# Kernel tuning notes

Hardware: AMD Instinct MI355X
Metric: run time of the kernel (lower is better)

The kernel has to match this reference:

```python
import jax, jax.numpy as jnp
import numpy as np

N_NODES = 50000
N_EDGES = 800000
IN_DIM = 128
OUT_DIM = 128
NEG_SLOPE = 0.01  # F.leaky_relu default


def setup_inputs() -> dict:
    key = jax.random.key(0)
    k_h, k_src, k_dst, k_w, k_as, k_ad = jax.random.split(key, 6)
    h = jax.random.normal(k_h, (N_NODES, IN_DIM), dtype=jnp.float32)
    src = jax.random.randint(k_src, (N_EDGES,), 0, N_NODES, dtype=jnp.int32)
    dst = jax.random.randint(k_dst, (N_EDGES,), 0, N_NODES, dtype=jnp.int32)
    # fc weight: xavier_normal with relu gain; stored as [in, out] for h @ W
    gain = float(np.sqrt(2.0))
    std_w = gain * np.sqrt(2.0 / (IN_DIM + OUT_DIM))
    W = jax.random.normal(k_w, (IN_DIM, OUT_DIM), dtype=jnp.float32) * std_w
    # attn weight [1, 2*out] split into src/dst halves (concat@a == z_s@a_s + z_d@a_d)
    std_a = gain * np.sqrt(2.0 / (2 * OUT_DIM + 1))
    a_src = jax.random.normal(k_as, (OUT_DIM,), dtype=jnp.float32) * std_a
    a_dst = jax.random.normal(k_ad, (OUT_DIM,), dtype=jnp.float32) * std_a
    return {"h": h, "src": src, "dst": dst, "W": W, "a_src": a_src, "a_dst": a_dst}


def reference(h, src, dst, W, a_src, a_dst):
    n = h.shape[0]
    z = h @ W                                   # [N, D]
    # edge attention: leaky_relu(attn(concat[z_src, z_dst]))
    e = z[src] @ a_src + z[dst] @ a_dst         # [E]
    e = jnp.where(e >= 0, e, NEG_SLOPE * e)
    # segment softmax over incoming edges of each dst node
    m = jax.ops.segment_max(e, dst, num_segments=n)    # [N]
    m = jnp.where(jnp.isfinite(m), m, 0.0)             # guard zero-in-degree nodes
    ex = jnp.exp(e - m[dst])                            # [E]
    denom = jax.ops.segment_sum(ex, dst, num_segments=n)
    denom = jnp.where(denom > 0, denom, 1.0)
    alpha = ex / denom[dst]                             # [E]
    # weighted scatter-sum of source features
    out = jax.ops.segment_sum(alpha[:, None] * z[src], dst, num_segments=n)  # [N, D]
    return out
```

## Files before the change

### kernel.cpp

```cpp
#include <hip/hip_runtime.h>
#include <math.h>

#define DIM 128
#define NEG_SLOPE 0.01f
#define CAP 64

typedef __attribute__((ext_vector_type(8))) short bf16x8;
typedef __attribute__((ext_vector_type(4))) float f32x4;
typedef unsigned int uint;
typedef unsigned short ushort;

static __device__ __forceinline__ uint f2bf(float x) {
  uint u = __float_as_uint(x);
  return (u + 0x7fffu + ((u >> 16) & 1u)) >> 16;
}

__global__ __launch_bounds__(256) void prep_fill(
    const float* __restrict__ W,
    const float* __restrict__ a_src, const float* __restrict__ a_dst,
    const float* __restrict__ h,
    const int* __restrict__ src, const int* __restrict__ dst,
    ushort* __restrict__ Wt16, float* __restrict__ s, float* __restrict__ d,
    int* __restrict__ cur, ushort* __restrict__ bucket,
    int n, int E, int nsd)
{
  __shared__ float vec[2][DIM];
  const int t = threadIdx.x;
  const int b = blockIdx.x;

  if (b == 0) {
    const float4* W4 = (const float4*)W;
    #pragma unroll
    for (int it = 0; it < 16; ++it) {
      int i = t + it * 256;
      int k = i >> 5, n4 = (i & 31) * 4;
      float4 v = W4[i];
      Wt16[(n4 + 0) * 128 + k] = (ushort)f2bf(v.x);
      Wt16[(n4 + 1) * 128 + k] = (ushort)f2bf(v.y);
      Wt16[(n4 + 2) * 128 + k] = (ushort)f2bf(v.z);
      Wt16[(n4 + 3) * 128 + k] = (ushort)f2bf(v.w);
    }
  } else if (b <= nsd) {
    {
      const float* row = W + (size_t)(t & 127) * DIM;
      const float* a = (t < 128) ? a_src : a_dst;
      float acc = 0.f;
      #pragma unroll 16
      for (int j = 0; j < DIM; ++j) acc = fmaf(row[j], a[j], acc);
      vec[t >> 7][t & 127] = acc;
    }
    __syncthreads();
    int i = (b - 1) * 256 + t;
    if (i < n) {
      const float4* h4 = (const float4*)(h + (size_t)i * DIM);
      float sp = 0.f, dp = 0.f;
      #pragma unroll 8
      for (int c = 0; c < 32; ++c) {
        float4 v = h4[c];
        sp = fmaf(v.x, vec[0][c*4+0], fmaf(v.y, vec[0][c*4+1],
             fmaf(v.z, vec[0][c*4+2], fmaf(v.w, vec[0][c*4+3], sp))));
        dp = fmaf(v.x, vec[1][c*4+0], fmaf(v.y, vec[1][c*4+1],
             fmaf(v.z, vec[1][c*4+2], fmaf(v.w, vec[1][c*4+3], dp))));
      }
      s[i] = sp; d[i] = dp;
    }
  } else {
    int i = (b - 1 - nsd) * 256 + t;
    if (i < E) {
      int sj = src[i], dj = dst[i];
      int c = atomicAdd(&cur[dj], 1);
      if (c < CAP)
        bucket[dj * CAP + c] = (ushort)sj;
    }
  }
}

__global__ __launch_bounds__(256) void gemm_mfma(
    const float* __restrict__ h, const ushort* __restrict__ Wt16,
    uint* __restrict__ zb,
    int n)
{
  __shared__ __align__(16) ushort hb[64 * 136];
  __shared__ __align__(16) ushort Wt[128 * 136];

  const int t = threadIdx.x;
  const int lane = t & 63, wv = t >> 6;
  const int row0 = blockIdx.x * 64;

  {
    const float4* h4 = (const float4*)h;
    #pragma unroll
    for (int it = 0; it < 8; ++it) {
      int i = t + it * 256;
      int r = i >> 5, c4 = i & 31;
      float4 v = make_float4(0.f, 0.f, 0.f, 0.f);
      if (row0 + r < n) v = h4[(size_t)(row0 + r) * 32 + c4];
      uint2 pk;
      pk.x = f2bf(v.x) | (f2bf(v.y) << 16);
      pk.y = f2bf(v.z) | (f2bf(v.w) << 16);
      *(uint2*)&hb[r * 136 + c4 * 4] = pk;
    }
  }
  {
    const uint4* Wg = (const uint4*)Wt16;
    #pragma unroll
    for (int it = 0; it < 8; ++it) {
      int i = t + it * 256;
      int nn = i >> 4, k8 = (i & 15) * 8;
      *(uint4*)&Wt[nn * 136 + k8] = Wg[i];
    }
  }
  __syncthreads();

  f32x4 acc[8];
  #pragma unroll
  for (int c = 0; c < 8; ++c) acc[c] = (f32x4){0.f, 0.f, 0.f, 0.f};

  const int m = lane & 15, quad = lane >> 4;
  const ushort* arow = &hb[(wv * 16 + m) * 136 + quad * 8];
  const ushort* brow = &Wt[m * 136 + quad * 8];

  #pragma unroll
  for (int ks = 0; ks < 4; ++ks) {
    bf16x8 af = *(const bf16x8*)(arow + ks * 32);
    #pragma unroll
    for (int c = 0; c < 8; ++c) {
      bf16x8 bf = *(const bf16x8*)(brow + c * 16 * 136 + ks * 32);
      acc[c] = __builtin_amdgcn_mfma_f32_16x16x32_bf16(af, bf, acc[c], 0, 0, 0);
    }
  }

  __syncthreads();
  #pragma unroll
  for (int c = 0; c < 8; ++c) {
    int col = c * 16 + m;
    #pragma unroll
    for (int reg = 0; reg < 4; ++reg) {
      int r = wv * 16 + quad * 4 + reg;
      hb[r * 136 + col] = (ushort)f2bf(acc[c][reg]);
    }
  }
  __syncthreads();
  #pragma unroll
  for (int it = 0; it < 4; ++it) {
    int i = t + it * 256;
    int r = i >> 4, c8 = i & 15;
    int rg = row0 + r;
    if (rg < n) {
      uint4 v = *(uint4*)&hb[r * 136 + c8 * 8];
      *(uint4*)&zb[(size_t)rg * 64 + c8 * 4] = v;
    }
  }
}

__global__ __launch_bounds__(256) void gat_node(
    const uint* __restrict__ zb, const float* __restrict__ s,
    const float* __restrict__ d, const int* __restrict__ cur,
    const ushort* __restrict__ bucket, float* __restrict__ out, int n)
{
  int wave = threadIdx.x >> 6;
  int lane = threadIdx.x & 63;
  int node = blockIdx.x * 4 + wave;
  if (node >= n) return;

  int cnt = min(cur[node], CAP);
  float2* out2 = (float2*)out;
  if (cnt <= 0) {
    out2[(size_t)node * 64 + lane] = make_float2(0.f, 0.f);
    return;
  }

  float dn = d[node];
  int sj = 0; float w = 0.f;
  if (lane < cnt) {
    sj = (int)bucket[node * CAP + lane];
    float e = s[sj] + dn;
    e = (e >= 0.f) ? e : NEG_SLOPE * e;
    w = __expf(e);
  }
  float denom = w;
  #pragma unroll
  for (int o = 32; o > 0; o >>= 1) denom += __shfl_xor(denom, o, 64);

  float2 acc = make_float2(0.f, 0.f);
  int tt = 0;
  for (; tt + 8 <= cnt; tt += 8) {
    uint zv[8]; float wt[8];
    #pragma unroll
    for (int u = 0; u < 8; ++u) {
      int st = __shfl(sj, tt + u, 64);
      zv[u] = zb[(size_t)st * 64 + lane];
      wt[u] = __shfl(w, tt + u, 64);
    }
    #pragma unroll
    for (int u = 0; u < 8; ++u) {
      acc.x = fmaf(wt[u], __uint_as_float(zv[u] << 16), acc.x);
      acc.y = fmaf(wt[u], __uint_as_float(zv[u] & 0xffff0000u), acc.y);
    }
  }
  for (; tt < cnt; ++tt) {
    int st = __shfl(sj, tt, 64);
    uint u = zb[(size_t)st * 64 + lane];
    float wt = __shfl(w, tt, 64);
    acc.x = fmaf(wt, __uint_as_float(u << 16), acc.x);
    acc.y = fmaf(wt, __uint_as_float(u & 0xffff0000u), acc.y);
  }
  float inv = 1.f / denom;
  out2[(size_t)node * 64 + lane] = make_float2(acc.x * inv, acc.y * inv);
}

extern "C" void kernel_launch(void* const* d_in, const int* in_sizes, int n_in,
                              void* d_out, int out_size, void* d_ws, size_t ws_size,
                              hipStream_t stream)
{
  const float* h     = (const float*)d_in[0];
  const int*   src   = (const int*)d_in[1];
  const int*   dst   = (const int*)d_in[2];
  const float* W     = (const float*)d_in[3];
  const float* a_src = (const float*)d_in[4];
  const float* a_dst = (const float*)d_in[5];
  float* out = (float*)d_out;

  const int n = in_sizes[0] / DIM;
  const int E = in_sizes[1];

  char* ws = (char*)d_ws;
  uint* zb       = (uint*)ws;   ws += (size_t)n * 64 * 4;
  float* s       = (float*)ws;  ws += (size_t)n * 4;
  float* d       = (float*)ws;  ws += (size_t)n * 4;
  int* cur       = (int*)ws;    ws += (size_t)n * 4;
  ushort* Wt16   = (ushort*)ws; ws += (size_t)DIM * DIM * 2;
  ushort* bucket = (ushort*)ws;

  const int nsd   = (n + 255) / 256;
  const int nfill = (E + 255) / 256;
  const int ngemm = (n + 63) / 64;

  hipMemsetAsync(cur, 0, (size_t)n * 4, stream);
  prep_fill<<<1 + nsd + nfill, 256, 0, stream>>>(
      W, a_src, a_dst, h, src, dst, Wt16, s, d, cur, bucket, n, E, nsd);
  gemm_mfma<<<ngemm, 256, 0, stream>>>(h, Wt16, zb, n);
  gat_node<<<(n + 3) / 4, 256, 0, stream>>>(zb, s, d, cur, bucket, out, n);
}
```

Before: 173.0 us.

## Fold memset into prep, merge bucket fill with GEMM, unroll gather deeper

The hipMemset of the in-degree counters is replaced by zeroing inside the prep kernel. The edge bucket fill moves into the GEMM launch as extra blocks, so the atomic scatter overlaps the MFMA work and one launch is removed. The GEMM now reads its B fragments straight from global memory instead of staging W in LDS, which cuts shared memory per block and raises occupancy at the cost of uncached-looking global loads. The gather loop in gat_node is unrolled to 16 neighbors so more loads are in flight.

```diff
diff --git a/kernel.cpp b/kernel.cpp
--- a/kernel.cpp
+++ b/kernel.cpp
@@ -15,14 +15,12 @@
   return (u + 0x7fffu + ((u >> 16) & 1u)) >> 16;
 }
 
-__global__ __launch_bounds__(256) void prep_fill(
+__global__ __launch_bounds__(256) void prep(
     const float* __restrict__ W,
     const float* __restrict__ a_src, const float* __restrict__ a_dst,
     const float* __restrict__ h,
-    const int* __restrict__ src, const int* __restrict__ dst,
     ushort* __restrict__ Wt16, float* __restrict__ s, float* __restrict__ d,
-    int* __restrict__ cur, ushort* __restrict__ bucket,
-    int n, int E, int nsd)
+    int* __restrict__ cur, int n, int nsd)
 {
   __shared__ float vec[2][DIM];
   const int t = threadIdx.x;
@@ -66,24 +64,31 @@
     }
   } else {
     int i = (b - 1 - nsd) * 256 + t;
+    if (i < n) cur[i] = 0;
+  }
+}
+
+__global__ __launch_bounds__(256) void fill_gemm(
+    const float* __restrict__ h, const ushort* __restrict__ Wt16,
+    const int* __restrict__ src, const int* __restrict__ dst,
+    int* __restrict__ cur, ushort* __restrict__ bucket,
+    uint* __restrict__ zb,
+    int n, int E, int ngemm)
+{
+  __shared__ __align__(16) ushort hb[64 * 136];
+  const int t = threadIdx.x;
+
+  if (blockIdx.x >= ngemm) {
+    int i = (blockIdx.x - ngemm) * 256 + t;
     if (i < E) {
       int sj = src[i], dj = dst[i];
       int c = atomicAdd(&cur[dj], 1);
       if (c < CAP)
         bucket[dj * CAP + c] = (ushort)sj;
     }
-  }
-}
-
-__global__ __launch_bounds__(256) void gemm_mfma(
-    const float* __restrict__ h, const ushort* __restrict__ Wt16,
-    uint* __restrict__ zb,
-    int n)
-{
-  __shared__ __align__(16) ushort hb[64 * 136];
-  __shared__ __align__(16) ushort Wt[128 * 136];
-
-  const int t = threadIdx.x;
+    return;
+  }
+
   const int lane = t & 63, wv = t >> 6;
   const int row0 = blockIdx.x * 64;
 
@@ -101,15 +106,6 @@
       *(uint2*)&hb[r * 136 + c4 * 4] = pk;
     }
   }
-  {
-    const uint4* Wg = (const uint4*)Wt16;
-    #pragma unroll
-    for (int it = 0; it < 8; ++it) {
-      int i = t + it * 256;
-      int nn = i >> 4, k8 = (i & 15) * 8;
-      *(uint4*)&Wt[nn * 136 + k8] = Wg[i];
-    }
-  }
   __syncthreads();
 
   f32x4 acc[8];
@@ -118,14 +114,14 @@
 
   const int m = lane & 15, quad = lane >> 4;
   const ushort* arow = &hb[(wv * 16 + m) * 136 + quad * 8];
-  const ushort* brow = &Wt[m * 136 + quad * 8];
+  const ushort* bbase = Wt16 + (size_t)m * 128 + quad * 8;
 
   #pragma unroll
   for (int ks = 0; ks < 4; ++ks) {
     bf16x8 af = *(const bf16x8*)(arow + ks * 32);
     #pragma unroll
     for (int c = 0; c < 8; ++c) {
-      bf16x8 bf = *(const bf16x8*)(brow + c * 16 * 136 + ks * 32);
+      bf16x8 bf = *(const bf16x8*)(bbase + c * 2048 + ks * 32);
       acc[c] = __builtin_amdgcn_mfma_f32_16x16x32_bf16(af, bf, acc[c], 0, 0, 0);
     }
   }
@@ -184,7 +180,21 @@
 
   float2 acc = make_float2(0.f, 0.f);
   int tt = 0;
-  for (; tt + 8 <= cnt; tt += 8) {
+  for (; tt + 16 <= cnt; tt += 16) {
+    uint zv[16]; float wt[16];
+    #pragma unroll
+    for (int u = 0; u < 16; ++u) {
+      int st = __shfl(sj, tt + u, 64);
+      zv[u] = zb[(size_t)st * 64 + lane];
+      wt[u] = __shfl(w, tt + u, 64);
+    }
+    #pragma unroll
+    for (int u = 0; u < 16; ++u) {
+      acc.x = fmaf(wt[u], __uint_as_float(zv[u] << 16), acc.x);
+      acc.y = fmaf(wt[u], __uint_as_float(zv[u] & 0xffff0000u), acc.y);
+    }
+  }
+  if (tt + 8 <= cnt) {
     uint zv[8]; float wt[8];
     #pragma unroll
     for (int u = 0; u < 8; ++u) {
@@ -197,6 +207,7 @@
       acc.x = fmaf(wt[u], __uint_as_float(zv[u] << 16), acc.x);
       acc.y = fmaf(wt[u], __uint_as_float(zv[u] & 0xffff0000u), acc.y);
     }
+    tt += 8;
   }
   for (; tt < cnt; ++tt) {
     int st = __shfl(sj, tt, 64);
@@ -233,12 +244,13 @@
   ushort* bucket = (ushort*)ws;
 
   const int nsd   = (n + 255) / 256;
+  const int ncur  = (n + 255) / 256;
   const int nfill = (E + 255) / 256;
   const int ngemm = (n + 63) / 64;
 
-  hipMemsetAsync(cur, 0, (size_t)n * 4, stream);
-  prep_fill<<<1 + nsd + nfill, 256, 0, stream>>>(
-      W, a_src, a_dst, h, src, dst, Wt16, s, d, cur, bucket, n, E, nsd);
-  gemm_mfma<<<ngemm, 256, 0, stream>>>(h, Wt16, zb, n);
+  prep<<<1 + nsd + ncur, 256, 0, stream>>>(
+      W, a_src, a_dst, h, Wt16, s, d, cur, n, nsd);
+  fill_gemm<<<ngemm + nfill, 256, 0, stream>>>(
+      h, Wt16, src, dst, cur, bucket, zb, n, E, ngemm);
   gat_node<<<(n + 3) / 4, 256, 0, stream>>>(zb, s, d, cur, bucket, out, n);
 }
```

After: 184.6 us. 1.07x slower.
